# Kernel optimization log

Hardware: AMD Instinct MI355X
Metric: run time of the kernel (lower is better)

Reference implementation:

```python
import jax, jax.numpy as jnp
import numpy as np

N_PAPER = 100000
N_AUTHOR = 50000
E = 800000
D_IN, D_HID, D_OUT = 128, 128, 64


def seg_max(x, src, dst, num_segments):
    # adj_t.matmul(x, reduce='max'): per-destination max over neighbor features;
    # destinations with no in-edges get 0 (torch_sparse convention).
    m = jax.ops.segment_max(x[src], dst, num_segments=num_segments)
    return jnp.where(jnp.isneginf(m), jnp.zeros((), m.dtype), m)


def setup_inputs() -> dict:
    key = jax.random.key(0)
    ks = jax.random.split(key, 32)
    inp = {}
    inp['x_paper'] = jax.random.normal(ks[0], (N_PAPER, D_IN), jnp.float32)
    inp['emb_author'] = jax.random.normal(ks[1], (N_AUTHOR, D_IN), jnp.float32)
    inp['writes_src'] = jax.random.randint(ks[2], (E,), 0, N_AUTHOR, jnp.int32)
    inp['writes_dst'] = jax.random.randint(ks[3], (E,), 0, N_PAPER, jnp.int32)
    inp['cites_src'] = jax.random.randint(ks[4], (E,), 0, N_PAPER, jnp.int32)
    inp['cites_dst'] = jax.random.randint(ks[5], (E,), 0, N_PAPER, jnp.int32)
    inp['wb_src'] = jax.random.randint(ks[6], (E,), 0, N_PAPER, jnp.int32)
    inp['wb_dst'] = jax.random.randint(ks[7], (E,), 0, N_AUTHOR, jnp.int32)

    def lin_w(k, din, dout):
        s = 1.0 / np.sqrt(din)
        return jax.random.uniform(k, (din, dout), jnp.float32, -s, s)

    # layer 1: D_IN -> D_HID
    inp['w1_rel_writes'] = lin_w(ks[8], D_IN, D_HID)
    inp['w1_rel_cites'] = lin_w(ks[9], D_IN, D_HID)
    inp['w1_rel_wb'] = lin_w(ks[10], D_IN, D_HID)
    inp['w1_root_paper'] = lin_w(ks[11], D_IN, D_HID)
    inp['b1_root_paper'] = jnp.zeros((D_HID,), jnp.float32)
    inp['w1_root_author'] = lin_w(ks[12], D_IN, D_HID)
    inp['b1_root_author'] = jnp.zeros((D_HID,), jnp.float32)
    # layer 2: D_HID -> D_OUT
    inp['w2_rel_writes'] = lin_w(ks[13], D_HID, D_OUT)
    inp['w2_rel_cites'] = lin_w(ks[14], D_HID, D_OUT)
    inp['w2_rel_wb'] = lin_w(ks[15], D_HID, D_OUT)
    inp['w2_root_paper'] = lin_w(ks[16], D_HID, D_OUT)
    inp['b2_root_paper'] = jnp.zeros((D_OUT,), jnp.float32)
    inp['w2_root_author'] = lin_w(ks[17], D_HID, D_OUT)
    inp['b2_root_author'] = jnp.zeros((D_OUT,), jnp.float32)
    return inp


def _conv(xp, xa, edges, w_writes, w_cites, w_wb, w_rp, b_rp, w_ra, b_ra):
    writes_src, writes_dst, cites_src, cites_dst, wb_src, wb_dst = edges
    out_p = xp @ w_rp + b_rp
    out_a = xa @ w_ra + b_ra
    out_p = out_p + seg_max(xa, writes_src, writes_dst, N_PAPER) @ w_writes
    out_p = out_p + seg_max(xp, cites_src, cites_dst, N_PAPER) @ w_cites
    out_a = out_a + seg_max(xp, wb_src, wb_dst, N_AUTHOR) @ w_wb
    return out_p, out_a


def reference(x_paper, emb_author,
              writes_src, writes_dst, cites_src, cites_dst, wb_src, wb_dst,
              w1_rel_writes, w1_rel_cites, w1_rel_wb,
              w1_root_paper, b1_root_paper, w1_root_author, b1_root_author,
              w2_rel_writes, w2_rel_cites, w2_rel_wb,
              w2_root_paper, b2_root_paper, w2_root_author, b2_root_author):
    edges = (writes_src, writes_dst, cites_src, cites_dst, wb_src, wb_dst)
    hp, ha = _conv(x_paper, emb_author, edges,
                   w1_rel_writes, w1_rel_cites, w1_rel_wb,
                   w1_root_paper, b1_root_paper, w1_root_author, b1_root_author)
    hp, ha = jax.nn.relu(hp), jax.nn.relu(ha)  # dropout p=0 -> identity
    return _conv(hp, ha, edges,
                 w2_rel_writes, w2_rel_cites, w2_rel_wb,
                 w2_root_paper, b2_root_paper, w2_root_author, b2_root_author)
```

## Files before the change

kernel.cpp:

```cpp
#include <hip/hip_runtime.h>


#define DI 128
#define NP 100000
#define NA 50000
#define EPB 4096
#define MAXBIN 391

typedef short s8v __attribute__((ext_vector_type(8)));
typedef float f32x4 __attribute__((ext_vector_type(4)));

__device__ __forceinline__ unsigned short bf16_rne(float f) {
  unsigned int fb = __float_as_uint(f);
  fb += 0x7FFFu + ((fb >> 16) & 1u);
  return (unsigned short)(fb >> 16);
}

__global__ __launch_bounds__(256) void cvt2_k(const float* __restrict__ Xp,
                                              unsigned short* __restrict__ Yp, int n4p,
                                              const float* __restrict__ Xa,
                                              unsigned short* __restrict__ Ya, int n4a) {
  int i = blockIdx.x * 256 + threadIdx.x;
  const float* X; unsigned short* Y;
  if (i < n4p) { X = Xp; Y = Yp; }
  else { i -= n4p; if (i >= n4a) return; X = Xa; Y = Ya; }
  float4 f = reinterpret_cast<const float4*>(X)[i];
  ushort4 o;
  o.x = bf16_rne(f.x); o.y = bf16_rne(f.y); o.z = bf16_rne(f.z); o.w = bf16_rne(f.w);
  reinterpret_cast<ushort4*>(Y)[i] = o;
}

struct R3Args {
  const int* src[3]; const int* dst[3];
  int* bh[3]; int* bhs[3];
  unsigned int* tmp[3];
  int* bkt[3]; int* cnt[3]; int* rs[3];
  int E[3]; int N[3]; int nbin[3]; int NB[3];
};

__global__ __launch_bounds__(256) void radix_s1_k(R3Args a) {
  int y = blockIdx.y, blk = blockIdx.x;
  int NB = a.NB[y];
  if (blk >= NB) return;
  __shared__ int hist[MAXBIN];
  int nbin = a.nbin[y];
  for (int i = threadIdx.x; i < nbin; i += 256) hist[i] = 0;
  __syncthreads();
  int e0 = blk * EPB, e1 = min(e0 + EPB, a.E[y]);
  const int* dst = a.dst[y];
  for (int e = e0 + threadIdx.x; e < e1; e += 256)
    atomicAdd(&hist[dst[e] >> 8], 1);
  __syncthreads();
  int* bh = a.bh[y];
  for (int i = threadIdx.x; i < nbin; i += 256) bh[i * NB + blk] = hist[i];
}

__global__ __launch_bounds__(256) void radix_x1_k(R3Args a) {
  int y = blockIdx.y, blk = blockIdx.x;
  int NB = a.NB[y];
  if (blk >= NB) return;
  __shared__ int cur[MAXBIN];
  int nbin = a.nbin[y];
  const int* bhs = a.bhs[y];
  for (int i = threadIdx.x; i < nbin; i += 256) cur[i] = bhs[i * NB + blk];
  __syncthreads();
  int e0 = blk * EPB, e1 = min(e0 + EPB, a.E[y]);
  const int* dst = a.dst[y];
  const int* src = a.src[y];
  unsigned int* tmp = a.tmp[y];
  for (int e = e0 + threadIdx.x; e < e1; e += 256) {
    int d = dst[e];
    int pos = atomicAdd(&cur[d >> 8], 1);
    tmp[pos] = ((unsigned int)(d & 255) << 24) | (unsigned int)src[e];
  }
}

__global__ __launch_bounds__(256) void radix_p2_k(R3Args a) {
  int y = blockIdx.y, bin = blockIdx.x;
  if (bin >= a.nbin[y]) return;
  __shared__ int hist[256], scn[256], cursor[256];
  int t = threadIdx.x;
  hist[t] = 0;
  __syncthreads();
  const int* bhs = a.bhs[y];
  int NB = a.NB[y];
  int base = bhs[bin * NB];
  int end  = (bin + 1 < a.nbin[y]) ? bhs[(bin + 1) * NB] : a.E[y];
  const unsigned int* tmp = a.tmp[y];
  for (int i = base + t; i < end; i += 256)
    atomicAdd(&hist[tmp[i] >> 24], 1);
  __syncthreads();
  int v = hist[t];
  scn[t] = v; __syncthreads();
  int acc = v;
  for (int o = 1; o < 256; o <<= 1) {
    int u = (t >= o) ? scn[t - o] : 0;
    __syncthreads();
    acc += u; scn[t] = acc;
    __syncthreads();
  }
  int ex = acc - v;
  cursor[t] = ex;
  int d = bin * 256 + t;
  if (d < a.N[y]) { a.cnt[y][d] = v; a.rs[y][d] = base + ex; }
  __syncthreads();
  int* bkt = a.bkt[y];
  for (int i = base + t; i < end; i += 256) {
    unsigned int p = tmp[i];
    int pos = atomicAdd(&cursor[p >> 24], 1);
    bkt[base + pos] = (int)(p & 0xFFFFFFu);
  }
}

struct S3Args {
  const int* cnt[3]; int* bsum[3]; int* rs[3];
  int n[3]; int nb[3];
};

__global__ __launch_bounds__(256) void blocksum3_k(S3Args a) {
  int y = blockIdx.y;
  int n = a.n[y];
  if (blockIdx.x * 1024 >= n) return;
  __shared__ int red[256];
  int t = threadIdx.x;
  int base = blockIdx.x * 1024 + t * 4;
  int s = 0;
  #pragma unroll
  for (int i = 0; i < 4; ++i) { int idx = base + i; if (idx < n) s += a.cnt[y][idx]; }
  red[t] = s; __syncthreads();
  #pragma unroll
  for (int o = 128; o > 0; o >>= 1) { if (t < o) red[t] += red[t + o]; __syncthreads(); }
  if (t == 0) a.bsum[y][blockIdx.x] = red[0];
}

__global__ __launch_bounds__(256) void partials3_k(S3Args a) {
  __shared__ int sm[256];
  int y = blockIdx.x;
  int nb = a.nb[y];
  int t = threadIdx.x;
  int v = (t < nb) ? a.bsum[y][t] : 0;
  sm[t] = v; __syncthreads();
  int acc = v;
  for (int o = 1; o < 256; o <<= 1) {
    int u = (t >= o) ? sm[t - o] : 0;
    __syncthreads();
    acc += u; sm[t] = acc;
    __syncthreads();
  }
  if (t < nb) a.bsum[y][t] = acc - v;
}

__global__ __launch_bounds__(256) void scanwrite3_k(S3Args a) {
  int y = blockIdx.y;
  int n = a.n[y];
  if (blockIdx.x * 1024 >= n) return;
  __shared__ int ts[256];
  int t = threadIdx.x;
  int base = blockIdx.x * 1024 + t * 4;
  int v[4]; int s = 0;
  #pragma unroll
  for (int i = 0; i < 4; ++i) { int idx = base + i; v[i] = (idx < n) ? a.cnt[y][idx] : 0; s += v[i]; }
  ts[t] = s; __syncthreads();
  int inc = s;
  for (int o = 1; o < 256; o <<= 1) {
    int u = (t >= o) ? ts[t - o] : 0;
    __syncthreads();
    inc += u; ts[t] = inc;
    __syncthreads();
  }
  int p = a.bsum[y][blockIdx.x] + inc - s;
  #pragma unroll
  for (int i = 0; i < 4; ++i) { int idx = base + i; if (idx < n) { a.rs[y][idx] = p; p += v[i]; } }
}

struct G3Args {
  const int* cnt[3]; const int* rs[3]; const int* bkt[3];
  const unsigned short* X[3]; unsigned short* S[3];
  int N[3];
};

__global__ __launch_bounds__(256) void gather3_k(G3Args a) {
  const int y = blockIdx.y;
  const int lane = threadIdx.x & 63;
  const int wave = threadIdx.x >> 6;
  const int g = lane >> 4, lg = lane & 15;
  const int d = blockIdx.x * 16 + wave * 4 + g;
  if (d >= a.N[y]) return;

  unsigned short* So = a.S[y] + (size_t)d * DI + lg * 8;
  const int deg = a.cnt[y][d];
  if (deg == 0) {
    uint4 z; z.x = z.y = z.z = z.w = 0u;
    *reinterpret_cast<uint4*>(So) = z;
    return;
  }
  const int* bp = a.bkt[y] + a.rs[y][d];
  const unsigned short* X = a.X[y];

  float ml[4], mh[4];
  #pragma unroll
  for (int j = 0; j < 4; ++j) { ml[j] = -3.4e38f; mh[j] = -3.4e38f; }

  int s0 = bp[0];
  for (int e = 0; e < deg; e += 2) {
    int s1 = (e + 1 < deg) ? bp[e + 1] : s0;
    int sn = (e + 2 < deg) ? bp[e + 2] : s0;
    uint4 r0 = *reinterpret_cast<const uint4*>(X + (size_t)s0 * DI + lg * 8);
    uint4 r1 = *reinterpret_cast<const uint4*>(X + (size_t)s1 * DI + lg * 8);
    unsigned int w0[4] = {r0.x, r0.y, r0.z, r0.w};
    unsigned int w1[4] = {r1.x, r1.y, r1.z, r1.w};
    #pragma unroll
    for (int j = 0; j < 4; ++j) {
      ml[j] = fmaxf(ml[j], __uint_as_float(w0[j] << 16));
      mh[j] = fmaxf(mh[j], __uint_as_float(w0[j] & 0xFFFF0000u));
      ml[j] = fmaxf(ml[j], __uint_as_float(w1[j] << 16));
      mh[j] = fmaxf(mh[j], __uint_as_float(w1[j] & 0xFFFF0000u));
    }
    s0 = sn;
  }
  uint4 o;
  o.x = (__float_as_uint(ml[0]) >> 16) | (__float_as_uint(mh[0]) & 0xFFFF0000u);
  o.y = (__float_as_uint(ml[1]) >> 16) | (__float_as_uint(mh[1]) & 0xFFFF0000u);
  o.z = (__float_as_uint(ml[2]) >> 16) | (__float_as_uint(mh[2]) & 0xFFFF0000u);
  o.w = (__float_as_uint(ml[3]) >> 16) | (__float_as_uint(mh[3]) & 0xFFFF0000u);
  *reinterpret_cast<uint4*>(So) = o;
}

struct WArgs {
  const float* w[10];
  unsigned short* wf[10];
};
__global__ __launch_bounds__(256) void warrange_k(WArgs args) {
  int widx = blockIdx.y;
  int OUTi = (widx < 5) ? 128 : 64;
  int CF = OUTi / 16;
  int nt = 4 * CF * 64;
  int t = blockIdx.x * 256 + threadIdx.x;
  if (t >= nt) return;
  int lane = t & 63, tmp = t >> 6;
  int cf = tmp % CF, kc = tmp / CF;
  int k0 = kc * 32 + (lane >> 4) * 8;
  int c  = cf * 16 + (lane & 15);
  const float* w = args.w[widx];
  s8v v;
  #pragma unroll
  for (int i = 0; i < 8; ++i) v[i] = (short)bf16_rne(w[(k0 + i) * OUTi + c]);
  *(reinterpret_cast<s8v*>(args.wf[widx]) + t) = v;
}

template<int CF>
__device__ __forceinline__ void mfma_accum(const unsigned short* __restrict__ A,
                                           const unsigned short* __restrict__ W,
                                           f32x4* acc, size_t arow, int lane, int half) {
  const s8v* a = reinterpret_cast<const s8v*>(A + arow * DI + half * 8);
  const s8v* w = reinterpret_cast<const s8v*>(W) + lane;
  #pragma unroll
  for (int kc = 0; kc < 4; ++kc) {
    s8v av = a[kc * 4];
    #pragma unroll
    for (int cf = 0; cf < CF; ++cf)
      acc[cf] = __builtin_amdgcn_mfma_f32_16x16x32_bf16(av, w[(kc * CF + cf) * 64], acc[cf], 0, 0, 0);
  }
}

struct GemmPairArgs {
  const unsigned short *A0[2], *W0[2], *A1[2], *W1[2], *A2, *W2;
  const float* bias[2];
  void* out[2];
  int N[2];
  int blocks0;
};

template<int OUT, bool RELU, bool OUT_BF16>
__global__ __launch_bounds__(256) void gemm_pair_k(GemmPairArgs g) {
  constexpr int CF = OUT / 16;
  const int p = (blockIdx.x >= (unsigned)g.blocks0) ? 1 : 0;
  const int brow = blockIdx.x - (p ? g.blocks0 : 0);
  const int N = g.N[p];
  const int lane = threadIdx.x & 63;
  const int wave = threadIdx.x >> 6;
  const int row0 = brow * 64 + wave * 16;
  if (row0 >= N) return;
  const int rl = lane & 15, half = lane >> 4;
  const size_t arow = (size_t)(row0 + rl);

  f32x4 acc[CF];
  #pragma unroll
  for (int i = 0; i < CF; ++i) acc[i] = f32x4{0.f, 0.f, 0.f, 0.f};

  mfma_accum<CF>(g.A0[p], g.W0[p], acc, arow, lane, half);
  mfma_accum<CF>(g.A1[p], g.W1[p], acc, arow, lane, half);
  if (!p) mfma_accum<CF>(g.A2, g.W2, acc, arow, lane, half);

  const float* bias = g.bias[p];
  #pragma unroll
  for (int cf = 0; cf < CF; ++cf) {
    float bv = bias[cf * 16 + rl];
    #pragma unroll
    for (int j = 0; j < 4; ++j) {
      int r = row0 + half * 4 + j;
      if (r >= N) continue;
      float v = acc[cf][j] + bv;
      if (RELU) v = v > 0.f ? v : 0.f;
      size_t idx = (size_t)r * OUT + cf * 16 + rl;
      if (OUT_BF16) ((unsigned short*)g.out[p])[idx] = bf16_rne(v);
      else          ((float*)g.out[p])[idx] = v;
    }
  }
}

extern "C" void kernel_launch(void* const* d_in, const int* in_sizes, int n_in,
                              void* d_out, int out_size, void* d_ws, size_t ws_size,
                              hipStream_t stream) {
  const float* xp = (const float*)d_in[0];
  const float* xa = (const float*)d_in[1];
  const int* wsrc = (const int*)d_in[2];
  const int* wdst = (const int*)d_in[3];
  const int* csrc = (const int*)d_in[4];
  const int* cdst = (const int*)d_in[5];
  const int* bsrc = (const int*)d_in[6];
  const int* bdst = (const int*)d_in[7];
  const int Ew = in_sizes[2], Ec = in_sizes[4], Eb = in_sizes[6];

  const float* w1w  = (const float*)d_in[8];
  const float* w1c  = (const float*)d_in[9];
  const float* w1wb = (const float*)d_in[10];
  const float* w1rp = (const float*)d_in[11];
  const float* b1rp = (const float*)d_in[12];
  const float* w1ra = (const float*)d_in[13];
  const float* b1ra = (const float*)d_in[14];
  const float* w2w  = (const float*)d_in[15];
  const float* w2c  = (const float*)d_in[16];
  const float* w2wb = (const float*)d_in[17];
  const float* w2rp = (const float*)d_in[18];
  const float* b2rp = (const float*)d_in[19];
  const float* w2ra = (const float*)d_in[20];
  const float* b2ra = (const float*)d_in[21];

  char* ws = (char*)d_ws;
  unsigned short* xpb = (unsigned short*)(ws + 0);
  unsigned short* xab = (unsigned short*)(ws + 25600000);
  unsigned short* hp  = (unsigned short*)(ws + 38400000);
  unsigned short* ha  = (unsigned short*)(ws + 64000000);
  unsigned short* S_w = (unsigned short*)(ws + 76800000);
  unsigned short* S_c = (unsigned short*)(ws + 102400000);
  unsigned short* S_b = (unsigned short*)(ws + 128000000);
  int* bkt_w = (int*)(ws + 140800000);
  int* bkt_c = (int*)(ws + 144000000);
  int* bkt_b = (int*)(ws + 147200000);
  int* cnt_w = (int*)(ws + 150400000);
  int* cnt_c = (int*)(ws + 150800000);
  int* cnt_b = (int*)(ws + 151200000);
  int* rs_w  = (int*)(ws + 151400000);
  int* rs_c  = (int*)(ws + 151800000);
  int* rs_b  = (int*)(ws + 152200000);
  int* bsum_w = (int*)(ws + 152400000);
  int* bsum_c = (int*)(ws + 152404096);
  int* bsum_b = (int*)(ws + 152408192);
  unsigned short* wf = (unsigned short*)(ws + 152412288);
  unsigned int* tmp_w = (unsigned int*)(ws + 152660000);
  unsigned int* tmp_c = (unsigned int*)(ws + 155860000);
  unsigned int* tmp_b = (unsigned int*)(ws + 159060000);
  int* bh_w  = (int*)(ws + 76800000);
  int* bh_c  = (int*)(ws + 77110000);
  int* bh_b  = (int*)(ws + 77420000);
  int* bhs_w = (int*)(ws + 77580000);
  int* bhs_c = (int*)(ws + 77890000);
  int* bhs_b = (int*)(ws + 78200000);

  unsigned short* WF[10];
  size_t off = 0;
  for (int i = 0; i < 10; ++i) {
    WF[i] = wf + off;
    off += (i < 5) ? (size_t)128 * 128 : (size_t)128 * 64;
  }
  WArgs wa;
  const float* wsrcs[10] = {w1w, w1c, w1wb, w1rp, w1ra, w2w, w2c, w2wb, w2rp, w2ra};
  for (int i = 0; i < 10; ++i) { wa.w[i] = wsrcs[i]; wa.wf[i] = WF[i]; }

  float* outP = (float*)d_out;
  float* outA = outP + (size_t)NP * 64;

  const int gP = (NP + 63) / 64, gA = (NA + 63) / 64;
  const int gG = (NP + 15) / 16;

  R3Args ra;
  ra.src[0] = wsrc; ra.dst[0] = wdst; ra.E[0] = Ew; ra.N[0] = NP;
  ra.src[1] = csrc; ra.dst[1] = cdst; ra.E[1] = Ec; ra.N[1] = NP;
  ra.src[2] = bsrc; ra.dst[2] = bdst; ra.E[2] = Eb; ra.N[2] = NA;
  ra.bh[0] = bh_w; ra.bh[1] = bh_c; ra.bh[2] = bh_b;
  ra.bhs[0] = bhs_w; ra.bhs[1] = bhs_c; ra.bhs[2] = bhs_b;
  ra.tmp[0] = tmp_w; ra.tmp[1] = tmp_c; ra.tmp[2] = tmp_b;
  ra.bkt[0] = bkt_w; ra.bkt[1] = bkt_c; ra.bkt[2] = bkt_b;
  ra.cnt[0] = cnt_w; ra.cnt[1] = cnt_c; ra.cnt[2] = cnt_b;
  ra.rs[0] = rs_w; ra.rs[1] = rs_c; ra.rs[2] = rs_b;
  int gSX = 0, gSC = 0, maxbin = 0;
  for (int y = 0; y < 3; ++y) {
    ra.nbin[y] = (ra.N[y] + 255) >> 8;
    ra.NB[y] = (ra.E[y] + EPB - 1) / EPB;
    if (ra.NB[y] > gSX) gSX = ra.NB[y];
    if (ra.nbin[y] > maxbin) maxbin = ra.nbin[y];
  }
  S3Args sa;
  sa.bsum[0] = bsum_w; sa.bsum[1] = bsum_c; sa.bsum[2] = bsum_b;
  for (int y = 0; y < 3; ++y) {
    sa.cnt[y] = ra.bh[y]; sa.rs[y] = ra.bhs[y];
    sa.n[y] = ra.nbin[y] * ra.NB[y];
    sa.nb[y] = (sa.n[y] + 1023) / 1024;
    if (sa.nb[y] > gSC) gSC = sa.nb[y];
  }

  G3Args g1, g2;
  for (int i = 0; i < 3; ++i) {
    g1.cnt[i] = g2.cnt[i] = (i == 0) ? cnt_w : (i == 1) ? cnt_c : cnt_b;
    g1.rs[i]  = g2.rs[i]  = (i == 0) ? rs_w  : (i == 1) ? rs_c  : rs_b;
    g1.bkt[i] = g2.bkt[i] = (i == 0) ? bkt_w : (i == 1) ? bkt_c : bkt_b;
    g1.S[i]   = g2.S[i]   = (i == 0) ? S_w   : (i == 1) ? S_c   : S_b;
    g1.N[i]   = g2.N[i]   = (i == 2) ? NA : NP;
  }
  g1.X[0] = xab; g1.X[1] = xpb; g1.X[2] = xpb;
  g2.X[0] = ha;  g2.X[1] = hp;  g2.X[2] = hp;

  GemmPairArgs p1, p2;
  p1.A0[0] = xpb; p1.W0[0] = WF[3]; p1.A1[0] = S_w; p1.W1[0] = WF[0]; p1.A2 = S_c; p1.W2 = WF[1];
  p1.bias[0] = b1rp; p1.out[0] = hp; p1.N[0] = NP;
  p1.A0[1] = xab; p1.W0[1] = WF[4]; p1.A1[1] = S_b; p1.W1[1] = WF[2];
  p1.bias[1] = b1ra; p1.out[1] = ha; p1.N[1] = NA;
  p1.blocks0 = gP;
  p2.A0[0] = hp; p2.W0[0] = WF[8]; p2.A1[0] = S_w; p2.W1[0] = WF[5]; p2.A2 = S_c; p2.W2 = WF[6];
  p2.bias[0] = b2rp; p2.out[0] = outP; p2.N[0] = NP;
  p2.A0[1] = ha; p2.W0[1] = WF[9]; p2.A1[1] = S_b; p2.W1[1] = WF[7];
  p2.bias[1] = b2ra; p2.out[1] = outA; p2.N[1] = NA;
  p2.blocks0 = gP;

  const int n4p = NP * DI / 4, n4a = NA * DI / 4;

  warrange_k<<<dim3(8, 10), 256, 0, stream>>>(wa);
  cvt2_k<<<(n4p + n4a + 255) / 256, 256, 0, stream>>>(xp, xpb, n4p, xa, xab, n4a);

  radix_s1_k<<<dim3(gSX, 3), 256, 0, stream>>>(ra);
  blocksum3_k<<<dim3(gSC, 3), 256, 0, stream>>>(sa);
  partials3_k<<<3, 256, 0, stream>>>(sa);
  scanwrite3_k<<<dim3(gSC, 3), 256, 0, stream>>>(sa);
  radix_x1_k<<<dim3(gSX, 3), 256, 0, stream>>>(ra);
  radix_p2_k<<<dim3(maxbin, 3), 256, 0, stream>>>(ra);

  gather3_k<<<dim3(gG, 3), 256, 0, stream>>>(g1);
  gemm_pair_k<128, true, true><<<gP + gA, 256, 0, stream>>>(p1);

  gather3_k<<<dim3(gG, 3), 256, 0, stream>>>(g2);
  gemm_pair_k<64, false, false><<<gP + gA, 256, 0, stream>>>(p2);
}
```

Measured before the change: 359.3 us.

## Fuse segment-max gather into per-layer MFMA GEMM via swizzled LDS tiles

Replaces the separate gather kernels and GEMM kernels with one fused kernel per layer. Each block gathers the max-aggregated neighbor rows for its 64 destinations straight into XOR-swizzled shared memory, then runs the MFMA products from LDS. This removes the write and re-read of the aggregated bf16 feature buffers and two launches. In exchange it uses 32KB of LDS per block, which lowers occupancy, and the latency-bound gather now sits serially before the MFMA work inside each block.

```diff
diff --git a/kernel.cpp b/kernel.cpp
--- a/kernel.cpp
+++ b/kernel.cpp
@@ -171,59 +171,6 @@
   int p = a.bsum[y][blockIdx.x] + inc - s;
   #pragma unroll
   for (int i = 0; i < 4; ++i) { int idx = base + i; if (idx < n) { a.rs[y][idx] = p; p += v[i]; } }
-}
-
-struct G3Args {
-  const int* cnt[3]; const int* rs[3]; const int* bkt[3];
-  const unsigned short* X[3]; unsigned short* S[3];
-  int N[3];
-};
-
-__global__ __launch_bounds__(256) void gather3_k(G3Args a) {
-  const int y = blockIdx.y;
-  const int lane = threadIdx.x & 63;
-  const int wave = threadIdx.x >> 6;
-  const int g = lane >> 4, lg = lane & 15;
-  const int d = blockIdx.x * 16 + wave * 4 + g;
-  if (d >= a.N[y]) return;
-
-  unsigned short* So = a.S[y] + (size_t)d * DI + lg * 8;
-  const int deg = a.cnt[y][d];
-  if (deg == 0) {
-    uint4 z; z.x = z.y = z.z = z.w = 0u;
-    *reinterpret_cast<uint4*>(So) = z;
-    return;
-  }
-  const int* bp = a.bkt[y] + a.rs[y][d];
-  const unsigned short* X = a.X[y];
-
-  float ml[4], mh[4];
-  #pragma unroll
-  for (int j = 0; j < 4; ++j) { ml[j] = -3.4e38f; mh[j] = -3.4e38f; }
-
-  int s0 = bp[0];
-  for (int e = 0; e < deg; e += 2) {
-    int s1 = (e + 1 < deg) ? bp[e + 1] : s0;
-    int sn = (e + 2 < deg) ? bp[e + 2] : s0;
-    uint4 r0 = *reinterpret_cast<const uint4*>(X + (size_t)s0 * DI + lg * 8);
-    uint4 r1 = *reinterpret_cast<const uint4*>(X + (size_t)s1 * DI + lg * 8);
-    unsigned int w0[4] = {r0.x, r0.y, r0.z, r0.w};
-    unsigned int w1[4] = {r1.x, r1.y, r1.z, r1.w};
-    #pragma unroll
-    for (int j = 0; j < 4; ++j) {
-      ml[j] = fmaxf(ml[j], __uint_as_float(w0[j] << 16));
-      mh[j] = fmaxf(mh[j], __uint_as_float(w0[j] & 0xFFFF0000u));
-      ml[j] = fmaxf(ml[j], __uint_as_float(w1[j] << 16));
-      mh[j] = fmaxf(mh[j], __uint_as_float(w1[j] & 0xFFFF0000u));
-    }
-    s0 = sn;
-  }
-  uint4 o;
-  o.x = (__float_as_uint(ml[0]) >> 16) | (__float_as_uint(mh[0]) & 0xFFFF0000u);
-  o.y = (__float_as_uint(ml[1]) >> 16) | (__float_as_uint(mh[1]) & 0xFFFF0000u);
-  o.z = (__float_as_uint(ml[2]) >> 16) | (__float_as_uint(mh[2]) & 0xFFFF0000u);
-  o.w = (__float_as_uint(ml[3]) >> 16) | (__float_as_uint(mh[3]) & 0xFFFF0000u);
-  *reinterpret_cast<uint4*>(So) = o;
 }
 
 struct WArgs {
@@ -248,10 +195,60 @@
   *(reinterpret_cast<s8v*>(args.wf[widx]) + t) = v;
 }
 
+
+__device__ __forceinline__ void gather_to_lds(
+    unsigned short* __restrict__ ldsT,
+    const int* __restrict__ cnt, const int* __restrict__ rs,
+    const int* __restrict__ bkt, const unsigned short* __restrict__ X,
+    int row0, int N)
+{
+  const int t = threadIdx.x;
+  const int lg = t & 15;
+  const int rr = t >> 4;
+  #pragma unroll
+  for (int pass = 0; pass < 4; ++pass) {
+    const int r = pass * 16 + rr;
+    const int d = row0 + r;
+    uint4 o; o.x = o.y = o.z = o.w = 0u;
+    if (d < N) {
+      const int deg = cnt[d];
+      if (deg > 0) {
+        const int* bp = bkt + rs[d];
+        float ml[4], mh[4];
+        #pragma unroll
+        for (int j = 0; j < 4; ++j) { ml[j] = -3.4e38f; mh[j] = -3.4e38f; }
+        int s0 = bp[0];
+        for (int e = 0; e < deg; e += 2) {
+          int s1 = (e + 1 < deg) ? bp[e + 1] : s0;
+          int sn = (e + 2 < deg) ? bp[e + 2] : s0;
+          uint4 r0 = *reinterpret_cast<const uint4*>(X + (size_t)s0 * DI + lg * 8);
+          uint4 r1 = *reinterpret_cast<const uint4*>(X + (size_t)s1 * DI + lg * 8);
+          unsigned int w0[4] = {r0.x, r0.y, r0.z, r0.w};
+          unsigned int w1[4] = {r1.x, r1.y, r1.z, r1.w};
+          #pragma unroll
+          for (int j = 0; j < 4; ++j) {
+            ml[j] = fmaxf(ml[j], __uint_as_float(w0[j] << 16));
+            mh[j] = fmaxf(mh[j], __uint_as_float(w0[j] & 0xFFFF0000u));
+            ml[j] = fmaxf(ml[j], __uint_as_float(w1[j] << 16));
+            mh[j] = fmaxf(mh[j], __uint_as_float(w1[j] & 0xFFFF0000u));
+          }
+          s0 = sn;
+        }
+        o.x = (__float_as_uint(ml[0]) >> 16) | (__float_as_uint(mh[0]) & 0xFFFF0000u);
+        o.y = (__float_as_uint(ml[1]) >> 16) | (__float_as_uint(mh[1]) & 0xFFFF0000u);
+        o.z = (__float_as_uint(ml[2]) >> 16) | (__float_as_uint(mh[2]) & 0xFFFF0000u);
+        o.w = (__float_as_uint(ml[3]) >> 16) | (__float_as_uint(mh[3]) & 0xFFFF0000u);
+      }
+    }
+    const int byte = (r * 256 + lg * 16) ^ ((r & 7) << 4);
+    *reinterpret_cast<uint4*>(reinterpret_cast<char*>(ldsT) + byte) = o;
+  }
+}
+
 template<int CF>
-__device__ __forceinline__ void mfma_accum(const unsigned short* __restrict__ A,
-                                           const unsigned short* __restrict__ W,
-                                           f32x4* acc, size_t arow, int lane, int half) {
+__device__ __forceinline__ void mfma_global(const unsigned short* __restrict__ A,
+                                            const unsigned short* __restrict__ W,
+                                            f32x4* acc, size_t arow, int lane, int half) {
   const s8v* a = reinterpret_cast<const s8v*>(A + arow * DI + half * 8);
   const s8v* w = reinterpret_cast<const s8v*>(W) + lane;
   #pragma unroll
@@ -263,8 +260,29 @@
   }
 }
 
-struct GemmPairArgs {
-  const unsigned short *A0[2], *W0[2], *A1[2], *W1[2], *A2, *W2;
+template<int CF>
+__device__ __forceinline__ void mfma_lds(const unsigned short* __restrict__ ldsT,
+                                         const unsigned short* __restrict__ W,
+                                         f32x4* acc, int wrow, int lane) {
+  const int rl = lane & 15, half = lane >> 4;
+  const int r = wrow + rl;
+  const s8v* w = reinterpret_cast<const s8v*>(W) + lane;
+  #pragma unroll
+  for (int kc = 0; kc < 4; ++kc) {
+    const int byte = (r * 256 + half * 16 + kc * 64) ^ ((r & 7) << 4);
+    s8v av = *reinterpret_cast<const s8v*>(reinterpret_cast<const char*>(ldsT) + byte);
+    #pragma unroll
+    for (int cf = 0; cf < CF; ++cf)
+      acc[cf] = __builtin_amdgcn_mfma_f32_16x16x32_bf16(av, w[(kc * CF + cf) * 64], acc[cf], 0, 0, 0);
+  }
+}
+
+struct FLArgs {
+  const unsigned short *root[2], *Wroot[2];
+  const unsigned short *feat1[2], *Wrel1[2];
+  const unsigned short *feat2,    *Wrel2;
+  const int *cnt1[2], *rs1[2], *bkt1[2];
+  const int *cnt2,    *rs2,    *bkt2;
   const float* bias[2];
   void* out[2];
   int N[2];
@@ -272,25 +290,35 @@
 };
 
 template<int OUT, bool RELU, bool OUT_BF16>
-__global__ __launch_bounds__(256) void gemm_pair_k(GemmPairArgs g) {
+__global__ __launch_bounds__(256) void fused_layer_k(FLArgs g) {
   constexpr int CF = OUT / 16;
+  __shared__ unsigned short lds1[64 * 128];
+  __shared__ unsigned short lds2[64 * 128];
+
   const int p = (blockIdx.x >= (unsigned)g.blocks0) ? 1 : 0;
   const int brow = blockIdx.x - (p ? g.blocks0 : 0);
   const int N = g.N[p];
+  const int row0 = brow * 64;
+  if (row0 >= N) return;
+
+  gather_to_lds(lds1, g.cnt1[p], g.rs1[p], g.bkt1[p], g.feat1[p], row0, N);
+  if (p == 0)
+    gather_to_lds(lds2, g.cnt2, g.rs2, g.bkt2, g.feat2, row0, N);
+  __syncthreads();
+
   const int lane = threadIdx.x & 63;
   const int wave = threadIdx.x >> 6;
-  const int row0 = brow * 64 + wave * 16;
-  if (row0 >= N) return;
+  const int wrow = wave * 16;
   const int rl = lane & 15, half = lane >> 4;
-  const size_t arow = (size_t)(row0 + rl);
+  const size_t arow = (size_t)(row0 + wrow + rl);
 
   f32x4 acc[CF];
   #pragma unroll
   for (int i = 0; i < CF; ++i) acc[i] = f32x4{0.f, 0.f, 0.f, 0.f};
 
-  mfma_accum<CF>(g.A0[p], g.W0[p], acc, arow, lane, half);
-  mfma_accum<CF>(g.A1[p], g.W1[p], acc, arow, lane, half);
-  if (!p) mfma_accum<CF>(g.A2, g.W2, acc, arow, lane, half);
+  mfma_global<CF>(g.root[p], g.Wroot[p], acc, arow, lane, half);
+  mfma_lds<CF>(lds1, g.Wrel1[p], acc, wrow, lane);
+  if (p == 0) mfma_lds<CF>(lds2, g.Wrel2, acc, wrow, lane);
 
   const float* bias = g.bias[p];
   #pragma unroll
@@ -298,7 +326,7 @@
     float bv = bias[cf * 16 + rl];
     #pragma unroll
     for (int j = 0; j < 4; ++j) {
-      int r = row0 + half * 4 + j;
+      int r = row0 + wrow + half * 4 + j;
       if (r >= N) continue;
       float v = acc[cf][j] + bv;
       if (RELU) v = v > 0.f ? v : 0.f;
@@ -342,9 +370,6 @@
   unsigned short* xab = (unsigned short*)(ws + 25600000);
   unsigned short* hp  = (unsigned short*)(ws + 38400000);
   unsigned short* ha  = (unsigned short*)(ws + 64000000);
-  unsigned short* S_w = (unsigned short*)(ws + 76800000);
-  unsigned short* S_c = (unsigned short*)(ws + 102400000);
-  unsigned short* S_b = (unsigned short*)(ws + 128000000);
   int* bkt_w = (int*)(ws + 140800000);
   int* bkt_c = (int*)(ws + 144000000);
   int* bkt_b = (int*)(ws + 147200000);
@@ -382,7 +407,6 @@
   float* outA = outP + (size_t)NP * 64;
 
   const int gP = (NP + 63) / 64, gA = (NA + 63) / 64;
-  const int gG = (NP + 15) / 16;
 
   R3Args ra;
   ra.src[0] = wsrc; ra.dst[0] = wdst; ra.E[0] = Ew; ra.N[0] = NP;
@@ -410,28 +434,29 @@
     if (sa.nb[y] > gSC) gSC = sa.nb[y];
   }
 
-  G3Args g1, g2;
-  for (int i = 0; i < 3; ++i) {
-    g1.cnt[i] = g2.cnt[i] = (i == 0) ? cnt_w : (i == 1) ? cnt_c : cnt_b;
-    g1.rs[i]  = g2.rs[i]  = (i == 0) ? rs_w  : (i == 1) ? rs_c  : rs_b;
-    g1.bkt[i] = g2.bkt[i] = (i == 0) ? bkt_w : (i == 1) ? bkt_c : bkt_b;
-    g1.S[i]   = g2.S[i]   = (i == 0) ? S_w   : (i == 1) ? S_c   : S_b;
-    g1.N[i]   = g2.N[i]   = (i == 2) ? NA : NP;
-  }
-  g1.X[0] = xab; g1.X[1] = xpb; g1.X[2] = xpb;
-  g2.X[0] = ha;  g2.X[1] = hp;  g2.X[2] = hp;
-
-  GemmPairArgs p1, p2;
-  p1.A0[0] = xpb; p1.W0[0] = WF[3]; p1.A1[0] = S_w; p1.W1[0] = WF[0]; p1.A2 = S_c; p1.W2 = WF[1];
-  p1.bias[0] = b1rp; p1.out[0] = hp; p1.N[0] = NP;
-  p1.A0[1] = xab; p1.W0[1] = WF[4]; p1.A1[1] = S_b; p1.W1[1] = WF[2];
-  p1.bias[1] = b1ra; p1.out[1] = ha; p1.N[1] = NA;
-  p1.blocks0 = gP;
-  p2.A0[0] = hp; p2.W0[0] = WF[8]; p2.A1[0] = S_w; p2.W1[0] = WF[5]; p2.A2 = S_c; p2.W2 = WF[6];
-  p2.bias[0] = b2rp; p2.out[0] = outP; p2.N[0] = NP;
-  p2.A0[1] = ha; p2.W0[1] = WF[9]; p2.A1[1] = S_b; p2.W1[1] = WF[7];
-  p2.bias[1] = b2ra; p2.out[1] = outA; p2.N[1] = NA;
-  p2.blocks0 = gP;
+  FLArgs f1, f2;
+  f1.root[0] = xpb; f1.Wroot[0] = WF[3];
+  f1.feat1[0] = xab; f1.Wrel1[0] = WF[0];
+  f1.cnt1[0] = cnt_w; f1.rs1[0] = rs_w; f1.bkt1[0] = bkt_w;
+  f1.feat2 = xpb; f1.Wrel2 = WF[1];
+  f1.cnt2 = cnt_c; f1.rs2 = rs_c; f1.bkt2 = bkt_c;
+  f1.bias[0] = b1rp; f1.out[0] = hp; f1.N[0] = NP;
+  f1.root[1] = xab; f1.Wroot[1] = WF[4];
+  f1.feat1[1] = xpb; f1.Wrel1[1] = WF[2];
+  f1.cnt1[1] = cnt_b; f1.rs1[1] = rs_b; f1.bkt1[1] = bkt_b;
+  f1.bias[1] = b1ra; f1.out[1] = ha; f1.N[1] = NA;
+  f1.blocks0 = gP;
+  f2.root[0] = hp; f2.Wroot[0] = WF[8];
+  f2.feat1[0] = ha; f2.Wrel1[0] = WF[5];
+  f2.cnt1[0] = cnt_w; f2.rs1[0] = rs_w; f2.bkt1[0] = bkt_w;
+  f2.feat2 = hp; f2.Wrel2 = WF[6];
+  f2.cnt2 = cnt_c; f2.rs2 = rs_c; f2.bkt2 = bkt_c;
+  f2.bias[0] = b2rp; f2.out[0] = outP; f2.N[0] = NP;
+  f2.root[1] = ha; f2.Wroot[1] = WF[9];
+  f2.feat1[1] = hp; f2.Wrel1[1] = WF[7];
+  f2.cnt1[1] = cnt_b; f2.rs1[1] = rs_b; f2.bkt1[1] = bkt_b;
+  f2.bias[1] = b2ra; f2.out[1] = outA; f2.N[1] = NA;
+  f2.blocks0 = gP;
 
   const int n4p = NP * DI / 4, n4a = NA * DI / 4;
 
@@ -445,9 +470,6 @@
   radix_x1_k<<<dim3(gSX, 3), 256, 0, stream>>>(ra);
   radix_p2_k<<<dim3(maxbin, 3), 256, 0, stream>>>(ra);
 
-  gather3_k<<<dim3(gG, 3), 256, 0, stream>>>(g1);
-  gemm_pair_k<128, true, true><<<gP + gA, 256, 0, stream>>>(p1);
-
-  gather3_k<<<dim3(gG, 3), 256, 0, stream>>>(g2);
-  gemm_pair_k<64, false, false><<<gP + gA, 256, 0, stream>>>(p2);
-}
+  fused_layer_k<128, true, true><<<gP + gA, 256, 0, stream>>>(f1);
+  fused_layer_k<64, false, false><<<gP + gA, 256, 0, stream>>>(f2);
+}
```

Result: slower. 393.2 us (+9.4%).
